# Optimization experiments

Measured on AMD Instinct MI355X. Metric: run time of the kernel, lower is better.

The kernel has to match this reference:

```python
import jax, jax.numpy as jnp
import numpy as np

EMBED_DIM = 1024
NUM_HEADS = 16
HEAD_DIM = EMBED_DIM // NUM_HEADS
BATCH = 2
SEQ = 2048


def setup_inputs() -> dict:
    key = jax.random.key(0)
    ks = jax.random.split(key, 10)
    s = 1.0 / np.sqrt(EMBED_DIM)
    inp = {
        "query": jax.random.normal(ks[0], (BATCH, SEQ, EMBED_DIM), jnp.float32),
        # Linear weights stored as [in, out] (y = x @ W + b)
        "wq": jax.random.normal(ks[1], (EMBED_DIM, EMBED_DIM), jnp.float32) * s,
        "bq": jnp.zeros((EMBED_DIM,), jnp.float32),
        "wk": jax.random.normal(ks[2], (EMBED_DIM, EMBED_DIM), jnp.float32) * s,
        "bk": jnp.zeros((EMBED_DIM,), jnp.float32),
        "wv": jax.random.normal(ks[3], (EMBED_DIM, EMBED_DIM), jnp.float32) * s,
        "bv": jnp.zeros((EMBED_DIM,), jnp.float32),
        "wo": jax.random.normal(ks[4], (EMBED_DIM, EMBED_DIM), jnp.float32) * s,
        "bo": jnp.zeros((EMBED_DIM,), jnp.float32),
        "temperature": jnp.float32(HEAD_DIM),  # learnable temperature, init = head_dim
    }
    return inp


def reference(query, wq, bq, wk, bk, wv, bv, wo, bo, temperature):
    B, S, E = query.shape
    # self-attention: key = value = query
    Q = (query @ wq + bq).reshape(B, S, NUM_HEADS, HEAD_DIM).transpose(0, 2, 1, 3)
    K = (query @ wk + bk).reshape(B, S, NUM_HEADS, HEAD_DIM).transpose(0, 2, 1, 3)
    V = (query @ wv + bv).reshape(B, S, NUM_HEADS, HEAD_DIM).transpose(0, 2, 1, 3)
    # squared Euclidean distances: ||q||^2 + ||k||^2 - 2<q,k>
    q_sq = jnp.sum(Q * Q, axis=-1, keepdims=True)          # (B,H,Sq,1)
    k_sq = jnp.sum(K * K, axis=-1, keepdims=True)          # (B,H,Sk,1)
    qk = jnp.einsum("bhqd,bhkd->bhqk", Q, K)
    d_sq = jnp.maximum(q_sq + jnp.swapaxes(k_sq, -2, -1) - 2.0 * qk, 0.0)
    attn = jax.nn.softmax(-d_sq / temperature, axis=-1)    # (B,H,Sq,Sk)
    out = jnp.einsum("bhqk,bhkd->bhqd", attn, V)
    out = out.transpose(0, 2, 1, 3).reshape(B, S, E)
    return out @ wo + bo
```

## Files before the change

kernel.cpp:

```cpp
#include <hip/hip_runtime.h>
#include <stdint.h>
#include <stddef.h>


#define LOG2E 1.44269504088896f

typedef __attribute__((ext_vector_type(8))) short bf16x8;
typedef __attribute__((ext_vector_type(4))) float f32x4;
typedef __attribute__((ext_vector_type(4))) unsigned short u16x4;
typedef __attribute__((ext_vector_type(8))) unsigned short u16x8;

__device__ __forceinline__ unsigned short f2b(float f) {
  union { float f; unsigned int u; } x; x.f = f;
  unsigned int u = x.u;
  u += 0x7fffu + ((u >> 16) & 1u);
  return (unsigned short)(u >> 16);
}
__device__ __forceinline__ float b2f(unsigned short s) {
  union { unsigned int u; float f; } x; x.u = ((unsigned int)s) << 16;
  return x.f;
}
__device__ __forceinline__ unsigned int fbits(float f) {
  union { float f; unsigned int u; } x; x.f = f; return x.u;
}

#define GLD_LDS(g, l) __builtin_amdgcn_global_load_lds( \
    (const __attribute__((address_space(1))) void*)(g), \
    (__attribute__((address_space(3))) void*)(l), 16, 0, 0)

__global__ void prep_kernel(const float* __restrict__ X,
                            const float* __restrict__ wq, const float* __restrict__ wk,
                            const float* __restrict__ wv, const float* __restrict__ wo,
                            unsigned short* __restrict__ Xb,
                            unsigned short* __restrict__ WTqkv, unsigned short* __restrict__ WTo) {
  int z = blockIdx.z;
  if (z == 4) {
    size_t base = ((size_t)(blockIdx.y * 16 + blockIdx.x)) * 16384;
    #pragma unroll
    for (int j = 0; j < 16; ++j) {
      size_t i = base + (size_t)(j * 256 + threadIdx.x) * 4;
      f32x4 v = *(const f32x4*)&X[i];
      u16x4 o;
      #pragma unroll
      for (int k = 0; k < 4; ++k) o[k] = f2b(v[k]);
      *(u16x4*)&Xb[i] = o;
    }
    return;
  }
  __shared__ float tile[64][65];
  const float* src = (z == 0) ? wq : (z == 1) ? wk : (z == 2) ? wv : wo;
  unsigned short* dst = (z < 3) ? (WTqkv + (size_t)z * 1024 * 1024) : WTo;
  int k0 = blockIdx.y * 64, n0 = blockIdx.x * 64;
  int rr = threadIdx.x >> 6, cc = threadIdx.x & 63;
  #pragma unroll
  for (int p = 0; p < 16; ++p) {
    int row = p * 4 + rr;
    tile[row][cc] = src[(size_t)(k0 + row) * 1024 + n0 + cc];
  }
  __syncthreads();
  #pragma unroll
  for (int p = 0; p < 16; ++p) {
    int row = p * 4 + rr;
    dst[(size_t)(n0 + row) * 1024 + k0 + cc] = f2b(tile[cc][row]);
  }
}

__global__ __launch_bounds__(256, 3) void gemm_qkv_kernel(
    const unsigned short* __restrict__ X, const unsigned short* __restrict__ WT,
    const float* __restrict__ bq, const float* __restrict__ bk, const float* __restrict__ bv,
    const float* __restrict__ temp,
    unsigned short* __restrict__ Qb, unsigned short* __restrict__ Kb,
    unsigned short* __restrict__ VTo, float* __restrict__ qs2, float* __restrict__ ks2) {
  __shared__ __align__(16) unsigned short smem[16896];
  unsigned short* As = smem;
  unsigned short* Bs = smem + 8192;
  const int t = threadIdx.x, w = t >> 6, lane = t & 63;
  const int r = lane & 15, q4 = lane >> 4;
  const int m0 = blockIdx.y * 128, n0 = blockIdx.x * 128;
  const int wr = (w >> 1) * 64, wc = (w & 1) * 64;
  const unsigned short* Xg = X + (size_t)m0 * 1024;
  const unsigned short* Wg = WT + (size_t)n0 * 1024;
  f32x4 acc[4][4] = {};
  for (int k0 = 0; k0 < 1024; k0 += 64) {
    #pragma unroll
    for (int g = 0; g < 4; ++g) {
      int slot = g * 256 + t;
      int kh = slot >> 9, row = (slot >> 2) & 127, ko = (slot & 3) * 8;
      GLD_LDS(Xg + (size_t)row * 1024 + k0 + kh * 32 + ko, &As[(g * 256 + w * 64) * 8]);
      GLD_LDS(Wg + (size_t)row * 1024 + k0 + kh * 32 + ko, &Bs[(g * 256 + w * 64) * 8]);
    }
    __syncthreads();
    #pragma unroll
    for (int kh = 0; kh < 2; ++kh) {
      bf16x8 af[4], bfr[4];
      #pragma unroll
      for (int mf = 0; mf < 4; ++mf)
        af[mf] = *(const bf16x8*)&As[kh * 4096 + (wr + mf * 16 + r) * 32 + q4 * 8];
      #pragma unroll
      for (int nf = 0; nf < 4; ++nf)
        bfr[nf] = *(const bf16x8*)&Bs[kh * 4096 + (wc + nf * 16 + r) * 32 + q4 * 8];
      #pragma unroll
      for (int mf = 0; mf < 4; ++mf)
        #pragma unroll
        for (int nf = 0; nf < 4; ++nf)
          acc[mf][nf] = __builtin_amdgcn_mfma_f32_16x16x32_bf16(af[mf], bfr[nf], acc[mf][nf], 0, 0, 0);
    }
    __syncthreads();
  }
  const int nblk = n0 >> 10;
  if (nblk < 2) {
    const float* bias = (nblk == 0) ? bq : bk;
    unsigned short* OutB = (nblk == 0) ? Qb : Kb;
    float* S2 = (nblk == 0) ? qs2 : ks2;
    const float sc = LOG2E / temp[0];
    const int nc0 = n0 & 1023;
    float s2a[4][4] = {};
    #pragma unroll
    for (int nf = 0; nf < 4; ++nf) {
      int n = nc0 + wc + nf * 16 + r;
      float bb = bias[n];
      #pragma unroll
      for (int mf = 0; mf < 4; ++mf) {
        int m = m0 + wr + mf * 16 + q4 * 4;
        f32x4 v = acc[mf][nf];
        #pragma unroll
        for (int i = 0; i < 4; ++i) {
          unsigned short os = f2b(v[i] + bb);
          OutB[(size_t)(m + i) * 1024 + n] = os;
          float xb = b2f(os);
          s2a[mf][i] += xb * xb;
        }
      }
    }
    #pragma unroll
    for (int mf = 0; mf < 4; ++mf)
      #pragma unroll
      for (int i = 0; i < 4; ++i) {
        float v = s2a[mf][i];
        v += __shfl_xor(v, 1, 64);
        v += __shfl_xor(v, 2, 64);
        v += __shfl_xor(v, 4, 64);
        v += __shfl_xor(v, 8, 64);
        s2a[mf][i] = v * sc;
      }
    if (r == 0) {
      int hh = (nc0 + wc) >> 6;
      #pragma unroll
      for (int mf = 0; mf < 4; ++mf) {
        int m = m0 + wr + mf * 16 + q4 * 4;
        int bb2 = m >> 11, ss = m & 2047;
        #pragma unroll
        for (int i = 0; i < 4; ++i)
          S2[(size_t)(bb2 * 16 + hh) * 2048 + ss + i] = s2a[mf][i];
      }
    }
  } else {
    unsigned short* Vt = smem;
    const int c0 = n0 - 2048;
    const int head = w & 1;
    #pragma unroll
    for (int nf = 0; nf < 4; ++nf) {
      int c = c0 + wc + nf * 16 + r;
      float bb = bv[c];
      int d = c & 63;
      #pragma unroll
      for (int mf = 0; mf < 4; ++mf) {
        int mloc = wr + mf * 16 + q4 * 4;
        int G = mloc >> 6;
        int k6 = mloc & 63;
        int pos = (k6 >> 5) * 32 + ((k6 & 15) >> 2) * 8 + ((k6 >> 4) & 1) * 4;
        f32x4 v = acc[mf][nf];
        u16x4 pk;
        #pragma unroll
        for (int i = 0; i < 4; ++i) pk[i] = f2b(v[i] + bb);
        *(u16x4*)&Vt[(head * 64 + d) * 132 + G * 64 + pos] = pk;
      }
    }
    __syncthreads();
    int row = t >> 1, ch = t & 1;
    int hd = row >> 6, dd = row & 63;
    int hglob = (c0 >> 6) + hd;
    int bb2 = m0 >> 11, s0 = m0 & 2047;
    unsigned short* dst = &VTo[((size_t)((bb2 * 16 + hglob) * 64 + dd)) * 2048 + s0 + ch * 64];
    const unsigned short* srcL = &Vt[(hd * 64 + dd) * 132 + ch * 64];
    #pragma unroll
    for (int k2 = 0; k2 < 16; ++k2)
      *(u16x4*)&dst[k2 * 4] = *(const u16x4*)&srcL[k2 * 4];
  }
}

__global__ __launch_bounds__(256, 2) void flash_kernel(
    const unsigned short* __restrict__ Qb, const unsigned short* __restrict__ Kb,
    const unsigned short* __restrict__ VT, const float* __restrict__ qs2,
    const float* __restrict__ ks2, const float* __restrict__ temp,
    unsigned short* __restrict__ AO) {
  __shared__ __align__(16) unsigned short Ks[2][64 * 64];
  __shared__ __align__(16) unsigned short Vs[2][64 * 64];
  const int t = threadIdx.x, w = t >> 6, lane = t & 63;
  const int r = lane & 15, q4 = lane >> 4;
  const int bh = blockIdx.y, b = bh >> 4, h = bh & 15;
  const int q0 = blockIdx.x * 128;
  const float cc = 2.0f * LOG2E / temp[0];

  bf16x8 qf[2][2];
  #pragma unroll
  for (int mf = 0; mf < 2; ++mf) {
    int sq = q0 + w * 32 + mf * 16 + r;
    const unsigned short* qp = Qb + (size_t)(b * 2048 + sq) * 1024 + h * 64;
    #pragma unroll
    for (int ks = 0; ks < 2; ++ks) qf[mf][ks] = *(const bf16x8*)(qp + ks * 32 + q4 * 8);
  }
  float qs_s[2];
  #pragma unroll
  for (int mf = 0; mf < 2; ++mf)
    qs_s[mf] = qs2[bh * 2048 + q0 + w * 32 + mf * 16 + r];

  f32x4 accO[2][4] = {};
  f32x4 lsum[2] = {};
  bf16x8 ones;
  #pragma unroll
  for (int j = 0; j < 8; ++j) ones[j] = (short)0x3F80;

  const unsigned short* Kg = Kb + ((size_t)b * 2048) * 1024 + h * 64;
  const unsigned short* Vg = VT + ((size_t)bh * 64) * 2048;
  const float* kqb = ks2 + bh * 2048;

  #pragma unroll
  for (int g = 0; g < 2; ++g) {
    int slot = g * 256 + t;
    int khalf = slot >> 8, key = (slot >> 2) & 63, ko = (slot & 3) * 8;
    GLD_LDS(Kg + (size_t)key * 1024 + khalf * 32 + ko, &Ks[0][slot * 8]);
    int dd = slot >> 3, pb = (slot & 7) ^ (dd & 7);
    GLD_LDS(Vg + (size_t)dd * 2048 + pb * 8, &Vs[0][slot * 8]);
  }
  f32x4 kq[4];
  #pragma unroll
  for (int kfm = 0; kfm < 4; ++kfm)
    kq[kfm] = *(const f32x4*)&kqb[kfm * 16 + q4 * 4];

  #pragma unroll 2
  for (int c = 0; c < 32; ++c) {
    const int buf = c & 1;
    __syncthreads();
    f32x4 kqn[4];
    if (c < 31) {
      #pragma unroll
      for (int g = 0; g < 2; ++g) {
        int slot = g * 256 + t;
        int khalf = slot >> 8, key = (slot >> 2) & 63, ko = (slot & 3) * 8;
        GLD_LDS(Kg + (size_t)((c + 1) * 64 + key) * 1024 + khalf * 32 + ko,
                &Ks[buf ^ 1][slot * 8]);
        int dd = slot >> 3, pb = (slot & 7) ^ (dd & 7);
        GLD_LDS(Vg + (size_t)dd * 2048 + (c + 1) * 64 + pb * 8,
                &Vs[buf ^ 1][slot * 8]);
      }
      #pragma unroll
      for (int kfm = 0; kfm < 4; ++kfm)
        kqn[kfm] = *(const f32x4*)&kqb[(c + 1) * 64 + kfm * 16 + q4 * 4];
    }

    f32x4 accST[4][2] = {};
    #pragma unroll
    for (int ks = 0; ks < 2; ++ks) {
      #pragma unroll
      for (int kfm = 0; kfm < 4; ++kfm) {
        bf16x8 ka = *(const bf16x8*)&Ks[buf][(ks * 64 + kfm * 16 + r) * 32 + q4 * 8];
        accST[kfm][0] = __builtin_amdgcn_mfma_f32_16x16x32_bf16(ka, qf[0][ks], accST[kfm][0], 0, 0, 0);
        accST[kfm][1] = __builtin_amdgcn_mfma_f32_16x16x32_bf16(ka, qf[1][ks], accST[kfm][1], 0, 0, 0);
      }
    }

    bf16x8 pf[2][2];
    #pragma unroll
    for (int cb = 0; cb < 2; ++cb) {
      #pragma unroll
      for (int mf = 0; mf < 2; ++mf) {
        unsigned int dw[4];
        #pragma unroll
        for (int half = 0; half < 2; ++half) {
          int kfm = cb * 2 + half;
          float pp[4];
          #pragma unroll
          for (int i = 0; i < 4; ++i) {
            float u = __builtin_fmaf(cc, accST[kfm][mf][i], -(kq[kfm][i] + qs_s[mf]));
            pp[i] = __builtin_amdgcn_exp2f(fminf(u, 0.f));
          }
          dw[half * 2 + 0] = (fbits(pp[0]) >> 16) | (fbits(pp[1]) & 0xFFFF0000u);
          dw[half * 2 + 1] = (fbits(pp[2]) >> 16) | (fbits(pp[3]) & 0xFFFF0000u);
        }
        union { unsigned int d[4]; bf16x8 v; } cv;
        cv.d[0] = dw[0]; cv.d[1] = dw[1]; cv.d[2] = dw[2]; cv.d[3] = dw[3];
        pf[cb][mf] = cv.v;
      }
    }

    #pragma unroll
    for (int cb = 0; cb < 2; ++cb) {
      #pragma unroll
      for (int mf = 0; mf < 2; ++mf)
        lsum[mf] = __builtin_amdgcn_mfma_f32_16x16x32_bf16(pf[cb][mf], ones, lsum[mf], 0, 0, 0);
      #pragma unroll
      for (int df = 0; df < 4; ++df) {
        int dloc = df * 16 + r;
        int un = dloc * 8 + ((cb * 4 + q4) ^ (dloc & 7));
        bf16x8 vb = *(const bf16x8*)&Vs[buf][un * 8];
        #pragma unroll
        for (int mf = 0; mf < 2; ++mf)
          accO[mf][df] = __builtin_amdgcn_mfma_f32_16x16x32_bf16(pf[cb][mf], vb, accO[mf][df], 0, 0, 0);
      }
    }
    if (c < 31) {
      #pragma unroll
      for (int kfm = 0; kfm < 4; ++kfm) kq[kfm] = kqn[kfm];
    }
  }
  #pragma unroll
  for (int mf = 0; mf < 2; ++mf) {
    float inv[4];
    #pragma unroll
    for (int i = 0; i < 4; ++i) inv[i] = 1.0f / lsum[mf][i];
    #pragma unroll
    for (int df = 0; df < 4; ++df) {
      int d = df * 16 + r;
      #pragma unroll
      for (int i = 0; i < 4; ++i) {
        int sq = q0 + w * 32 + mf * 16 + q4 * 4 + i;
        AO[(size_t)(b * 2048 + sq) * 1024 + h * 64 + d] = f2b(accO[mf][df][i] * inv[i]);
      }
    }
  }
}

__global__ __launch_bounds__(256, 2) void gemm_out_kernel(
    const unsigned short* __restrict__ A, const unsigned short* __restrict__ WT,
    const float* __restrict__ bo, float* __restrict__ Out) {
  __shared__ __align__(16) unsigned short As[2 * 128 * 32];
  __shared__ __align__(16) unsigned short Bs[2 * 64 * 32];
  const int t = threadIdx.x, w = t >> 6, lane = t & 63;
  const int r = lane & 15, q4 = lane >> 4;
  const int m0 = blockIdx.y * 128, n0 = blockIdx.x * 64;
  const int wr = (w >> 1) * 64, wc = (w & 1) * 32;
  const unsigned short* Ag = A + (size_t)m0 * 1024;
  const unsigned short* Wg = WT + (size_t)n0 * 1024;
  f32x4 acc[4][2] = {};
  for (int k0 = 0; k0 < 1024; k0 += 64) {
    #pragma unroll
    for (int g = 0; g < 4; ++g) {
      int slot = g * 256 + t;
      int kh = slot >> 9, row = (slot >> 2) & 127, ko = (slot & 3) * 8;
      GLD_LDS(Ag + (size_t)row * 1024 + k0 + kh * 32 + ko, &As[(g * 256 + w * 64) * 8]);
    }
    #pragma unroll
    for (int g = 0; g < 2; ++g) {
      int slot = g * 256 + t;
      int kh = slot >> 8, row = (slot >> 2) & 63, ko = (slot & 3) * 8;
      GLD_LDS(Wg + (size_t)row * 1024 + k0 + kh * 32 + ko, &Bs[(g * 256 + w * 64) * 8]);
    }
    __syncthreads();
    #pragma unroll
    for (int kh = 0; kh < 2; ++kh) {
      bf16x8 af[4], bfr[2];
      #pragma unroll
      for (int mf = 0; mf < 4; ++mf)
        af[mf] = *(const bf16x8*)&As[kh * 4096 + (wr + mf * 16 + r) * 32 + q4 * 8];
      #pragma unroll
      for (int nf = 0; nf < 2; ++nf)
        bfr[nf] = *(const bf16x8*)&Bs[kh * 2048 + (wc + nf * 16 + r) * 32 + q4 * 8];
      #pragma unroll
      for (int mf = 0; mf < 4; ++mf)
        #pragma unroll
        for (int nf = 0; nf < 2; ++nf)
          acc[mf][nf] = __builtin_amdgcn_mfma_f32_16x16x32_bf16(af[mf], bfr[nf], acc[mf][nf], 0, 0, 0);
    }
    __syncthreads();
  }
  #pragma unroll
  for (int nf = 0; nf < 2; ++nf) {
    int n = n0 + wc + nf * 16 + r;
    float bb = bo[n];
    #pragma unroll
    for (int mf = 0; mf < 4; ++mf) {
      int m = m0 + wr + mf * 16 + q4 * 4;
      f32x4 v = acc[mf][nf];
      #pragma unroll
      for (int i = 0; i < 4; ++i)
        Out[(size_t)(m + i) * 1024 + n] = v[i] + bb;
    }
  }
}

extern "C" void kernel_launch(void* const* d_in, const int* in_sizes, int n_in,
                              void* d_out, int out_size, void* d_ws, size_t ws_size,
                              hipStream_t stream) {
  const float* X    = (const float*)d_in[0];
  const float* wq   = (const float*)d_in[1];
  const float* bq   = (const float*)d_in[2];
  const float* wk   = (const float*)d_in[3];
  const float* bk   = (const float*)d_in[4];
  const float* wv   = (const float*)d_in[5];
  const float* bv   = (const float*)d_in[6];
  const float* wo   = (const float*)d_in[7];
  const float* bo   = (const float*)d_in[8];
  const float* temp = (const float*)d_in[9];
  float* Out = (float*)d_out;

  char* ws = (char*)d_ws;
  unsigned short* Xb    = (unsigned short*)ws; ws += (size_t)4096 * 1024 * 2;
  unsigned short* WTqkv = (unsigned short*)ws; ws += (size_t)3072 * 1024 * 2;
  unsigned short* WTo   = (unsigned short*)ws; ws += (size_t)1024 * 1024 * 2;
  unsigned short* Qb    = (unsigned short*)ws; ws += (size_t)4096 * 1024 * 2;
  unsigned short* Kb    = (unsigned short*)ws; ws += (size_t)4096 * 1024 * 2;
  unsigned short* VT    = (unsigned short*)ws; ws += (size_t)4096 * 1024 * 2;
  float* qs2 = (float*)ws; ws += (size_t)65536 * 4;
  float* ks2 = (float*)ws; ws += (size_t)65536 * 4;
  unsigned short* AO = Xb;

  prep_kernel<<<dim3(16, 16, 5), 256, 0, stream>>>(X, wq, wk, wv, wo, Xb, WTqkv, WTo);
  gemm_qkv_kernel<<<dim3(24, 32), 256, 0, stream>>>(Xb, WTqkv, bq, bk, bv, temp, Qb, Kb, VT, qs2, ks2);
  flash_kernel<<<dim3(16, 32), 256, 0, stream>>>(Qb, Kb, VT, qs2, ks2, temp, AO);
  gemm_out_kernel<<<dim3(16, 32), 256, 0, stream>>>(AO, WTo, bo, Out);
}
```

Before: 203.2 us.

## Double-buffer GEMM k-loops and drop per-row q-norm term from softmax

The QKV and output projection GEMMs now use a double-buffered LDS pipeline with 32-wide k-steps and a single barrier per step, prefetching the next tile during compute. The per-query squared norm is dropped because it is constant across keys and cancels in the softmax, which removes the qs2 buffer, its loads and the clamp before exp2. The flash kernel load addressing is simplified to incrementing pointers. Removing the clamp relies on exponents staying bounded, and skipping the row-max subtraction could overflow for larger-magnitude inputs.

```diff
diff --git a/kernel.cpp b/kernel.cpp
--- a/kernel.cpp
+++ b/kernel.cpp
@@ -8,7 +8,6 @@
 typedef __attribute__((ext_vector_type(8))) short bf16x8;
 typedef __attribute__((ext_vector_type(4))) float f32x4;
 typedef __attribute__((ext_vector_type(4))) unsigned short u16x4;
-typedef __attribute__((ext_vector_type(8))) unsigned short u16x8;
 
 __device__ __forceinline__ unsigned short f2b(float f) {
   union { float f; unsigned int u; } x; x.f = f;
@@ -70,7 +69,7 @@
     const float* __restrict__ bq, const float* __restrict__ bk, const float* __restrict__ bv,
     const float* __restrict__ temp,
     unsigned short* __restrict__ Qb, unsigned short* __restrict__ Kb,
-    unsigned short* __restrict__ VTo, float* __restrict__ qs2, float* __restrict__ ks2) {
+    unsigned short* __restrict__ VTo, float* __restrict__ ks2) {
   __shared__ __align__(16) unsigned short smem[16896];
   unsigned short* As = smem;
   unsigned short* Bs = smem + 8192;
@@ -80,45 +79,63 @@
   const int wr = (w >> 1) * 64, wc = (w & 1) * 64;
   const unsigned short* Xg = X + (size_t)m0 * 1024;
   const unsigned short* Wg = WT + (size_t)n0 * 1024;
+  const unsigned short* xp0 = Xg + (size_t)(t >> 2) * 1024 + (t & 3) * 8;
+  const unsigned short* xp1 = xp0 + (size_t)64 * 1024;
+  const unsigned short* wp0 = Wg + (size_t)(t >> 2) * 1024 + (t & 3) * 8;
+  const unsigned short* wp1 = wp0 + (size_t)64 * 1024;
   f32x4 acc[4][4] = {};
-  for (int k0 = 0; k0 < 1024; k0 += 64) {
-    #pragma unroll
-    for (int g = 0; g < 4; ++g) {
-      int slot = g * 256 + t;
-      int kh = slot >> 9, row = (slot >> 2) & 127, ko = (slot & 3) * 8;
-      GLD_LDS(Xg + (size_t)row * 1024 + k0 + kh * 32 + ko, &As[(g * 256 + w * 64) * 8]);
-      GLD_LDS(Wg + (size_t)row * 1024 + k0 + kh * 32 + ko, &Bs[(g * 256 + w * 64) * 8]);
-    }
+  GLD_LDS(xp0, &As[t * 8]);
+  GLD_LDS(xp1, &As[(256 + t) * 8]);
+  GLD_LDS(wp0, &Bs[t * 8]);
+  GLD_LDS(wp1, &Bs[(256 + t) * 8]);
+  #pragma unroll 2
+  for (int kk = 0; kk < 32; ++kk) {
+    const int buf = kk & 1;
     __syncthreads();
-    #pragma unroll
-    for (int kh = 0; kh < 2; ++kh) {
-      bf16x8 af[4], bfr[4];
-      #pragma unroll
-      for (int mf = 0; mf < 4; ++mf)
-        af[mf] = *(const bf16x8*)&As[kh * 4096 + (wr + mf * 16 + r) * 32 + q4 * 8];
+    if (kk < 31) {
+      int ko = (kk + 1) * 32;
+      GLD_LDS(xp0 + ko, &As[(buf ^ 1) * 4096 + t * 8]);
+      GLD_LDS(xp1 + ko, &As[(buf ^ 1) * 4096 + (256 + t) * 8]);
+      GLD_LDS(wp0 + ko, &Bs[(buf ^ 1) * 4096 + t * 8]);
+      GLD_LDS(wp1 + ko, &Bs[(buf ^ 1) * 4096 + (256 + t) * 8]);
+    }
+    bf16x8 af[4], bfr[4];
+    #pragma unroll
+    for (int mf = 0; mf < 4; ++mf)
+      af[mf] = *(const bf16x8*)&As[buf * 4096 + (wr + mf * 16 + r) * 32 + q4 * 8];
+    #pragma unroll
+    for (int nf = 0; nf < 4; ++nf)
+      bfr[nf] = *(const bf16x8*)&Bs[buf * 4096 + (wc + nf * 16 + r) * 32 + q4 * 8];
+    #pragma unroll
+    for (int mf = 0; mf < 4; ++mf)
       #pragma unroll
       for (int nf = 0; nf < 4; ++nf)
-        bfr[nf] = *(const bf16x8*)&Bs[kh * 4096 + (wc + nf * 16 + r) * 32 + q4 * 8];
-      #pragma unroll
-      for (int mf = 0; mf < 4; ++mf)
-        #pragma unroll
-        for (int nf = 0; nf < 4; ++nf)
-          acc[mf][nf] = __builtin_amdgcn_mfma_f32_16x16x32_bf16(af[mf], bfr[nf], acc[mf][nf], 0, 0, 0);
-    }
-    __syncthreads();
+        acc[mf][nf] = __builtin_amdgcn_mfma_f32_16x16x32_bf16(af[mf], bfr[nf], acc[mf][nf], 0, 0, 0);
   }
   const int nblk = n0 >> 10;
-  if (nblk < 2) {
-    const float* bias = (nblk == 0) ? bq : bk;
-    unsigned short* OutB = (nblk == 0) ? Qb : Kb;
-    float* S2 = (nblk == 0) ? qs2 : ks2;
+  if (nblk == 0) {
+    const int nc0 = n0 & 1023;
+    #pragma unroll
+    for (int nf = 0; nf < 4; ++nf) {
+      int n = nc0 + wc + nf * 16 + r;
+      float bb = bq[n];
+      #pragma unroll
+      for (int mf = 0; mf < 4; ++mf) {
+        int m = m0 + wr + mf * 16 + q4 * 4;
+        f32x4 v = acc[mf][nf];
+        #pragma unroll
+        for (int i = 0; i < 4; ++i)
+          Qb[(size_t)(m + i) * 1024 + n] = f2b(v[i] + bb);
+      }
+    }
+  } else if (nblk == 1) {
     const float sc = LOG2E / temp[0];
     const int nc0 = n0 & 1023;
     float s2a[4][4] = {};
     #pragma unroll
     for (int nf = 0; nf < 4; ++nf) {
       int n = nc0 + wc + nf * 16 + r;
-      float bb = bias[n];
+      float bb = bk[n];
       #pragma unroll
       for (int mf = 0; mf < 4; ++mf) {
         int m = m0 + wr + mf * 16 + q4 * 4;
@@ -126,7 +143,7 @@
         #pragma unroll
         for (int i = 0; i < 4; ++i) {
           unsigned short os = f2b(v[i] + bb);
-          OutB[(size_t)(m + i) * 1024 + n] = os;
+          Kb[(size_t)(m + i) * 1024 + n] = os;
           float xb = b2f(os);
           s2a[mf][i] += xb * xb;
         }
@@ -151,10 +168,11 @@
         int bb2 = m >> 11, ss = m & 2047;
         #pragma unroll
         for (int i = 0; i < 4; ++i)
-          S2[(size_t)(bb2 * 16 + hh) * 2048 + ss + i] = s2a[mf][i];
+          ks2[(size_t)(bb2 * 16 + hh) * 2048 + ss + i] = s2a[mf][i];
       }
     }
   } else {
+    __syncthreads();
     unsigned short* Vt = smem;
     const int c0 = n0 - 2048;
     const int head = w & 1;
@@ -191,9 +209,8 @@
 
 __global__ __launch_bounds__(256, 2) void flash_kernel(
     const unsigned short* __restrict__ Qb, const unsigned short* __restrict__ Kb,
-    const unsigned short* __restrict__ VT, const float* __restrict__ qs2,
-    const float* __restrict__ ks2, const float* __restrict__ temp,
-    unsigned short* __restrict__ AO) {
+    const unsigned short* __restrict__ VT, const float* __restrict__ ks2,
+    const float* __restrict__ temp, unsigned short* __restrict__ AO) {
   __shared__ __align__(16) unsigned short Ks[2][64 * 64];
   __shared__ __align__(16) unsigned short Vs[2][64 * 64];
   const int t = threadIdx.x, w = t >> 6, lane = t & 63;
@@ -210,10 +227,6 @@
     #pragma unroll
     for (int ks = 0; ks < 2; ++ks) qf[mf][ks] = *(const bf16x8*)(qp + ks * 32 + q4 * 8);
   }
-  float qs_s[2];
-  #pragma unroll
-  for (int mf = 0; mf < 2; ++mf)
-    qs_s[mf] = qs2[bh * 2048 + q0 + w * 32 + mf * 16 + r];
 
   f32x4 accO[2][4] = {};
   f32x4 lsum[2] = {};
@@ -225,39 +238,32 @@
   const unsigned short* Vg = VT + ((size_t)bh * 64) * 2048;
   const float* kqb = ks2 + bh * 2048;
 
-  #pragma unroll
-  for (int g = 0; g < 2; ++g) {
-    int slot = g * 256 + t;
-    int khalf = slot >> 8, key = (slot >> 2) & 63, ko = (slot & 3) * 8;
-    GLD_LDS(Kg + (size_t)key * 1024 + khalf * 32 + ko, &Ks[0][slot * 8]);
-    int dd = slot >> 3, pb = (slot & 7) ^ (dd & 7);
-    GLD_LDS(Vg + (size_t)dd * 2048 + pb * 8, &Vs[0][slot * 8]);
-  }
-  f32x4 kq[4];
-  #pragma unroll
-  for (int kfm = 0; kfm < 4; ++kfm)
-    kq[kfm] = *(const f32x4*)&kqb[kfm * 16 + q4 * 4];
+  const unsigned short* kp0 = Kg + (size_t)(t >> 2) * 1024 + (t & 3) * 8;
+  const unsigned short* kp1 = kp0 + 32;
+  int dd0 = t >> 3;
+  const unsigned short* vp0 = Vg + (size_t)dd0 * 2048 + ((t & 7) ^ (dd0 & 7)) * 8;
+  const unsigned short* vp1 = vp0 + (size_t)32 * 2048;
+  GLD_LDS(kp0, &Ks[0][t * 8]);
+  GLD_LDS(kp1, &Ks[0][(256 + t) * 8]);
+  GLD_LDS(vp0, &Vs[0][t * 8]);
+  GLD_LDS(vp1, &Vs[0][(256 + t) * 8]);
+  kp0 += 65536; kp1 += 65536; vp0 += 64; vp1 += 64;
 
   #pragma unroll 2
   for (int c = 0; c < 32; ++c) {
     const int buf = c & 1;
     __syncthreads();
-    f32x4 kqn[4];
     if (c < 31) {
-      #pragma unroll
-      for (int g = 0; g < 2; ++g) {
-        int slot = g * 256 + t;
-        int khalf = slot >> 8, key = (slot >> 2) & 63, ko = (slot & 3) * 8;
-        GLD_LDS(Kg + (size_t)((c + 1) * 64 + key) * 1024 + khalf * 32 + ko,
-                &Ks[buf ^ 1][slot * 8]);
-        int dd = slot >> 3, pb = (slot & 7) ^ (dd & 7);
-        GLD_LDS(Vg + (size_t)dd * 2048 + (c + 1) * 64 + pb * 8,
-                &Vs[buf ^ 1][slot * 8]);
-      }
-      #pragma unroll
-      for (int kfm = 0; kfm < 4; ++kfm)
-        kqn[kfm] = *(const f32x4*)&kqb[(c + 1) * 64 + kfm * 16 + q4 * 4];
-    }
+      GLD_LDS(kp0, &Ks[buf ^ 1][t * 8]);
+      GLD_LDS(kp1, &Ks[buf ^ 1][(256 + t) * 8]);
+      GLD_LDS(vp0, &Vs[buf ^ 1][t * 8]);
+      GLD_LDS(vp1, &Vs[buf ^ 1][(256 + t) * 8]);
+      kp0 += 65536; kp1 += 65536; vp0 += 64; vp1 += 64;
+    }
+    f32x4 kq[4];
+    #pragma unroll
+    for (int kfm = 0; kfm < 4; ++kfm)
+      kq[kfm] = *(const f32x4*)&kqb[c * 64 + kfm * 16 + q4 * 4];
 
     f32x4 accST[4][2] = {};
     #pragma unroll
@@ -282,8 +288,8 @@
           float pp[4];
           #pragma unroll
           for (int i = 0; i < 4; ++i) {
-            float u = __builtin_fmaf(cc, accST[kfm][mf][i], -(kq[kfm][i] + qs_s[mf]));
-            pp[i] = __builtin_amdgcn_exp2f(fminf(u, 0.f));
+            float u = __builtin_fmaf(cc, accST[kfm][mf][i], -kq[kfm][i]);
+            pp[i] = __builtin_amdgcn_exp2f(u);
           }
           dw[half * 2 + 0] = (fbits(pp[0]) >> 16) | (fbits(pp[1]) & 0xFFFF0000u);
           dw[half * 2 + 1] = (fbits(pp[2]) >> 16) | (fbits(pp[3]) & 0xFFFF0000u);
@@ -309,10 +315,6 @@
           accO[mf][df] = __builtin_amdgcn_mfma_f32_16x16x32_bf16(pf[cb][mf], vb, accO[mf][df], 0, 0, 0);
       }
     }
-    if (c < 31) {
-      #pragma unroll
-      for (int kfm = 0; kfm < 4; ++kfm) kq[kfm] = kqn[kfm];
-    }
   }
   #pragma unroll
   for (int mf = 0; mf < 2; ++mf) {
@@ -334,45 +336,43 @@
 __global__ __launch_bounds__(256, 2) void gemm_out_kernel(
     const unsigned short* __restrict__ A, const unsigned short* __restrict__ WT,
     const float* __restrict__ bo, float* __restrict__ Out) {
-  __shared__ __align__(16) unsigned short As[2 * 128 * 32];
-  __shared__ __align__(16) unsigned short Bs[2 * 64 * 32];
+  __shared__ __align__(16) unsigned short As[2][128 * 32];
+  __shared__ __align__(16) unsigned short Bs[2][64 * 32];
   const int t = threadIdx.x, w = t >> 6, lane = t & 63;
   const int r = lane & 15, q4 = lane >> 4;
   const int m0 = blockIdx.y * 128, n0 = blockIdx.x * 64;
   const int wr = (w >> 1) * 64, wc = (w & 1) * 32;
   const unsigned short* Ag = A + (size_t)m0 * 1024;
   const unsigned short* Wg = WT + (size_t)n0 * 1024;
+  const unsigned short* ap0 = Ag + (size_t)(t >> 2) * 1024 + (t & 3) * 8;
+  const unsigned short* ap1 = ap0 + (size_t)64 * 1024;
+  const unsigned short* wp0 = Wg + (size_t)(t >> 2) * 1024 + (t & 3) * 8;
   f32x4 acc[4][2] = {};
-  for (int k0 = 0; k0 < 1024; k0 += 64) {
-    #pragma unroll
-    for (int g = 0; g < 4; ++g) {
-      int slot = g * 256 + t;
-      int kh = slot >> 9, row = (slot >> 2) & 127, ko = (slot & 3) * 8;
-      GLD_LDS(Ag + (size_t)row * 1024 + k0 + kh * 32 + ko, &As[(g * 256 + w * 64) * 8]);
-    }
-    #pragma unroll
-    for (int g = 0; g < 2; ++g) {
-      int slot = g * 256 + t;
-      int kh = slot >> 8, row = (slot >> 2) & 63, ko = (slot & 3) * 8;
-      GLD_LDS(Wg + (size_t)row * 1024 + k0 + kh * 32 + ko, &Bs[(g * 256 + w * 64) * 8]);
-    }
+  GLD_LDS(ap0, &As[0][t * 8]);
+  GLD_LDS(ap1, &As[0][(256 + t) * 8]);
+  GLD_LDS(wp0, &Bs[0][t * 8]);
+  #pragma unroll 2
+  for (int kk = 0; kk < 32; ++kk) {
+    const int buf = kk & 1;
     __syncthreads();
-    #pragma unroll
-    for (int kh = 0; kh < 2; ++kh) {
-      bf16x8 af[4], bfr[2];
-      #pragma unroll
-      for (int mf = 0; mf < 4; ++mf)
-        af[mf] = *(const bf16x8*)&As[kh * 4096 + (wr + mf * 16 + r) * 32 + q4 * 8];
+    if (kk < 31) {
+      int ko = (kk + 1) * 32;
+      GLD_LDS(ap0 + ko, &As[buf ^ 1][t * 8]);
+      GLD_LDS(ap1 + ko, &As[buf ^ 1][(256 + t) * 8]);
+      GLD_LDS(wp0 + ko, &Bs[buf ^ 1][t * 8]);
+    }
+    bf16x8 af[4], bfr[2];
+    #pragma unroll
+    for (int mf = 0; mf < 4; ++mf)
+      af[mf] = *(const bf16x8*)&As[buf][(wr + mf * 16 + r) * 32 + q4 * 8];
+    #pragma unroll
+    for (int nf = 0; nf < 2; ++nf)
+      bfr[nf] = *(const bf16x8*)&Bs[buf][(wc + nf * 16 + r) * 32 + q4 * 8];
+    #pragma unroll
+    for (int mf = 0; mf < 4; ++mf)
       #pragma unroll
       for (int nf = 0; nf < 2; ++nf)
-        bfr[nf] = *(const bf16x8*)&Bs[kh * 2048 + (wc + nf * 16 + r) * 32 + q4 * 8];
-      #pragma unroll
-      for (int mf = 0; mf < 4; ++mf)
-        #pragma unroll
-        for (int nf = 0; nf < 2; ++nf)
-          acc[mf][nf] = __builtin_amdgcn_mfma_f32_16x16x32_bf16(af[mf], bfr[nf], acc[mf][nf], 0, 0, 0);
-    }
-    __syncthreads();
+        acc[mf][nf] = __builtin_amdgcn_mfma_f32_16x16x32_bf16(af[mf], bfr[nf], acc[mf][nf], 0, 0, 0);
   }
   #pragma unroll
   for (int nf = 0; nf < 2; ++nf) {
@@ -411,12 +411,11 @@
   unsigned short* Qb    = (unsigned short*)ws; ws += (size_t)4096 * 1024 * 2;
   unsigned short* Kb    = (unsigned short*)ws; ws += (size_t)4096 * 1024 * 2;
   unsigned short* VT    = (unsigned short*)ws; ws += (size_t)4096 * 1024 * 2;
-  float* qs2 = (float*)ws; ws += (size_t)65536 * 4;
   float* ks2 = (float*)ws; ws += (size_t)65536 * 4;
   unsigned short* AO = Xb;
 
   prep_kernel<<<dim3(16, 16, 5), 256, 0, stream>>>(X, wq, wk, wv, wo, Xb, WTqkv, WTo);
-  gemm_qkv_kernel<<<dim3(24, 32), 256, 0, stream>>>(Xb, WTqkv, bq, bk, bv, temp, Qb, Kb, VT, qs2, ks2);
-  flash_kernel<<<dim3(16, 32), 256, 0, stream>>>(Qb, Kb, VT, qs2, ks2, temp, AO);
+  gemm_qkv_kernel<<<dim3(24, 32), 256, 0, stream>>>(Xb, WTqkv, bq, bk, bv, temp, Qb, Kb, VT, ks2);
+  flash_kernel<<<dim3(16, 32), 256, 0, stream>>>(Qb, Kb, VT, ks2, temp, AO);
   gemm_out_kernel<<<dim3(16, 32), 256, 0, stream>>>(AO, WTo, bo, Out);
 }
```

Measured after the change: 207.5 us. +2.1%, slower.

## Load K/V tiles straight to registers and drop the query-norm softmax term

Applied to the files above, without the earlier changes.

The flash kernel no longer stages K and V tiles in double-buffered LDS with barriers. Each wave now reads its K and V MFMA fragments directly from global memory into registers, which removes the syncthreads and LDS traffic but makes the four waves in a block fetch the same data redundantly. Separately, the per-query squared-norm term is dropped from the exponent, relying on softmax shift invariance, and the clamp to non-positive values is removed. The QKV GEMM therefore no longer computes or stores q_sq. Without that term and the clamp, the exponent is no longer bounded above, so overflow protection now depends on the input scale.

```diff
diff --git a/kernel.cpp b/kernel.cpp
--- a/kernel.cpp
+++ b/kernel.cpp
@@ -8,7 +8,6 @@
 typedef __attribute__((ext_vector_type(8))) short bf16x8;
 typedef __attribute__((ext_vector_type(4))) float f32x4;
 typedef __attribute__((ext_vector_type(4))) unsigned short u16x4;
-typedef __attribute__((ext_vector_type(8))) unsigned short u16x8;
 
 __device__ __forceinline__ unsigned short f2b(float f) {
   union { float f; unsigned int u; } x; x.f = f;
@@ -70,7 +69,7 @@
     const float* __restrict__ bq, const float* __restrict__ bk, const float* __restrict__ bv,
     const float* __restrict__ temp,
     unsigned short* __restrict__ Qb, unsigned short* __restrict__ Kb,
-    unsigned short* __restrict__ VTo, float* __restrict__ qs2, float* __restrict__ ks2) {
+    unsigned short* __restrict__ VTo, float* __restrict__ ks2) {
   __shared__ __align__(16) unsigned short smem[16896];
   unsigned short* As = smem;
   unsigned short* Bs = smem + 8192;
@@ -108,17 +107,29 @@
     __syncthreads();
   }
   const int nblk = n0 >> 10;
-  if (nblk < 2) {
-    const float* bias = (nblk == 0) ? bq : bk;
-    unsigned short* OutB = (nblk == 0) ? Qb : Kb;
-    float* S2 = (nblk == 0) ? qs2 : ks2;
+  if (nblk == 0) {
+    const int nc0 = n0 & 1023;
+    #pragma unroll
+    for (int nf = 0; nf < 4; ++nf) {
+      int n = nc0 + wc + nf * 16 + r;
+      float bb = bq[n];
+      #pragma unroll
+      for (int mf = 0; mf < 4; ++mf) {
+        int m = m0 + wr + mf * 16 + q4 * 4;
+        f32x4 v = acc[mf][nf];
+        #pragma unroll
+        for (int i = 0; i < 4; ++i)
+          Qb[(size_t)(m + i) * 1024 + n] = f2b(v[i] + bb);
+      }
+    }
+  } else if (nblk == 1) {
     const float sc = LOG2E / temp[0];
     const int nc0 = n0 & 1023;
     float s2a[4][4] = {};
     #pragma unroll
     for (int nf = 0; nf < 4; ++nf) {
       int n = nc0 + wc + nf * 16 + r;
-      float bb = bias[n];
+      float bb = bk[n];
       #pragma unroll
       for (int mf = 0; mf < 4; ++mf) {
         int m = m0 + wr + mf * 16 + q4 * 4;
@@ -126,7 +137,7 @@
         #pragma unroll
         for (int i = 0; i < 4; ++i) {
           unsigned short os = f2b(v[i] + bb);
-          OutB[(size_t)(m + i) * 1024 + n] = os;
+          Kb[(size_t)(m + i) * 1024 + n] = os;
           float xb = b2f(os);
           s2a[mf][i] += xb * xb;
         }
@@ -151,7 +162,7 @@
         int bb2 = m >> 11, ss = m & 2047;
         #pragma unroll
         for (int i = 0; i < 4; ++i)
-          S2[(size_t)(bb2 * 16 + hh) * 2048 + ss + i] = s2a[mf][i];
+          ks2[(size_t)(bb2 * 16 + hh) * 2048 + ss + i] = s2a[mf][i];
       }
     }
   } else {
@@ -191,11 +202,8 @@
 
 __global__ __launch_bounds__(256, 2) void flash_kernel(
     const unsigned short* __restrict__ Qb, const unsigned short* __restrict__ Kb,
-    const unsigned short* __restrict__ VT, const float* __restrict__ qs2,
-    const float* __restrict__ ks2, const float* __restrict__ temp,
-    unsigned short* __restrict__ AO) {
-  __shared__ __align__(16) unsigned short Ks[2][64 * 64];
-  __shared__ __align__(16) unsigned short Vs[2][64 * 64];
+    const unsigned short* __restrict__ VT, const float* __restrict__ ks2,
+    const float* __restrict__ temp, unsigned short* __restrict__ AO) {
   const int t = threadIdx.x, w = t >> 6, lane = t & 63;
   const int r = lane & 15, q4 = lane >> 4;
   const int bh = blockIdx.y, b = bh >> 4, h = bh & 15;
@@ -210,10 +218,6 @@
     #pragma unroll
     for (int ks = 0; ks < 2; ++ks) qf[mf][ks] = *(const bf16x8*)(qp + ks * 32 + q4 * 8);
   }
-  float qs_s[2];
-  #pragma unroll
-  for (int mf = 0; mf < 2; ++mf)
-    qs_s[mf] = qs2[bh * 2048 + q0 + w * 32 + mf * 16 + r];
 
   f32x4 accO[2][4] = {};
   f32x4 lsum[2] = {};
@@ -221,52 +225,38 @@
   #pragma unroll
   for (int j = 0; j < 8; ++j) ones[j] = (short)0x3F80;
 
-  const unsigned short* Kg = Kb + ((size_t)b * 2048) * 1024 + h * 64;
-  const unsigned short* Vg = VT + ((size_t)bh * 64) * 2048;
-  const float* kqb = ks2 + bh * 2048;
-
-  #pragma unroll
-  for (int g = 0; g < 2; ++g) {
-    int slot = g * 256 + t;
-    int khalf = slot >> 8, key = (slot >> 2) & 63, ko = (slot & 3) * 8;
-    GLD_LDS(Kg + (size_t)key * 1024 + khalf * 32 + ko, &Ks[0][slot * 8]);
-    int dd = slot >> 3, pb = (slot & 7) ^ (dd & 7);
-    GLD_LDS(Vg + (size_t)dd * 2048 + pb * 8, &Vs[0][slot * 8]);
-  }
-  f32x4 kq[4];
-  #pragma unroll
-  for (int kfm = 0; kfm < 4; ++kfm)
-    kq[kfm] = *(const f32x4*)&kqb[kfm * 16 + q4 * 4];
+  const unsigned short* kp0 = Kb + ((size_t)b * 2048 + r) * 1024 + h * 64 + q4 * 8;
+  const unsigned short* kp1 = kp0 + 16 * 1024;
+  const unsigned short* kp2 = kp0 + 32 * 1024;
+  const unsigned short* kp3 = kp0 + 48 * 1024;
+  const unsigned short* vp0 = VT + ((size_t)bh * 64 + r) * 2048 + q4 * 8;
+  const unsigned short* vp1 = vp0 + (size_t)16 * 2048;
+  const unsigned short* vp2 = vp0 + (size_t)32 * 2048;
+  const unsigned short* vp3 = vp0 + (size_t)48 * 2048;
+  const float* kqp = ks2 + bh * 2048 + q4 * 4;
 
   #pragma unroll 2
   for (int c = 0; c < 32; ++c) {
-    const int buf = c & 1;
-    __syncthreads();
-    f32x4 kqn[4];
-    if (c < 31) {
-      #pragma unroll
-      for (int g = 0; g < 2; ++g) {
-        int slot = g * 256 + t;
-        int khalf = slot >> 8, key = (slot >> 2) & 63, ko = (slot & 3) * 8;
-        GLD_LDS(Kg + (size_t)((c + 1) * 64 + key) * 1024 + khalf * 32 + ko,
-                &Ks[buf ^ 1][slot * 8]);
-        int dd = slot >> 3, pb = (slot & 7) ^ (dd & 7);
-        GLD_LDS(Vg + (size_t)dd * 2048 + (c + 1) * 64 + pb * 8,
-                &Vs[buf ^ 1][slot * 8]);
-      }
-      #pragma unroll
-      for (int kfm = 0; kfm < 4; ++kfm)
-        kqn[kfm] = *(const f32x4*)&kqb[(c + 1) * 64 + kfm * 16 + q4 * 4];
-    }
+    bf16x8 ka[2][4], vb[2][4];
+    ka[0][0] = *(const bf16x8*)(kp0);      ka[1][0] = *(const bf16x8*)(kp0 + 32);
+    ka[0][1] = *(const bf16x8*)(kp1);      ka[1][1] = *(const bf16x8*)(kp1 + 32);
+    ka[0][2] = *(const bf16x8*)(kp2);      ka[1][2] = *(const bf16x8*)(kp2 + 32);
+    ka[0][3] = *(const bf16x8*)(kp3);      ka[1][3] = *(const bf16x8*)(kp3 + 32);
+    vb[0][0] = *(const bf16x8*)(vp0);      vb[1][0] = *(const bf16x8*)(vp0 + 32);
+    vb[0][1] = *(const bf16x8*)(vp1);      vb[1][1] = *(const bf16x8*)(vp1 + 32);
+    vb[0][2] = *(const bf16x8*)(vp2);      vb[1][2] = *(const bf16x8*)(vp2 + 32);
+    vb[0][3] = *(const bf16x8*)(vp3);      vb[1][3] = *(const bf16x8*)(vp3 + 32);
+    f32x4 kq[4];
+    #pragma unroll
+    for (int kfm = 0; kfm < 4; ++kfm) kq[kfm] = *(const f32x4*)(kqp + kfm * 16);
 
     f32x4 accST[4][2] = {};
     #pragma unroll
     for (int ks = 0; ks < 2; ++ks) {
       #pragma unroll
       for (int kfm = 0; kfm < 4; ++kfm) {
-        bf16x8 ka = *(const bf16x8*)&Ks[buf][(ks * 64 + kfm * 16 + r) * 32 + q4 * 8];
-        accST[kfm][0] = __builtin_amdgcn_mfma_f32_16x16x32_bf16(ka, qf[0][ks], accST[kfm][0], 0, 0, 0);
-        accST[kfm][1] = __builtin_amdgcn_mfma_f32_16x16x32_bf16(ka, qf[1][ks], accST[kfm][1], 0, 0, 0);
+        accST[kfm][0] = __builtin_amdgcn_mfma_f32_16x16x32_bf16(ka[ks][kfm], qf[0][ks], accST[kfm][0], 0, 0, 0);
+        accST[kfm][1] = __builtin_amdgcn_mfma_f32_16x16x32_bf16(ka[ks][kfm], qf[1][ks], accST[kfm][1], 0, 0, 0);
       }
     }
 
@@ -282,8 +272,8 @@
           float pp[4];
           #pragma unroll
           for (int i = 0; i < 4; ++i) {
-            float u = __builtin_fmaf(cc, accST[kfm][mf][i], -(kq[kfm][i] + qs_s[mf]));
-            pp[i] = __builtin_amdgcn_exp2f(fminf(u, 0.f));
+            float u = __builtin_fmaf(cc, accST[kfm][mf][i], -kq[kfm][i]);
+            pp[i] = __builtin_amdgcn_exp2f(u);
           }
           dw[half * 2 + 0] = (fbits(pp[0]) >> 16) | (fbits(pp[1]) & 0xFFFF0000u);
           dw[half * 2 + 1] = (fbits(pp[2]) >> 16) | (fbits(pp[3]) & 0xFFFF0000u);
@@ -301,18 +291,14 @@
         lsum[mf] = __builtin_amdgcn_mfma_f32_16x16x32_bf16(pf[cb][mf], ones, lsum[mf], 0, 0, 0);
       #pragma unroll
       for (int df = 0; df < 4; ++df) {
-        int dloc = df * 16 + r;
-        int un = dloc * 8 + ((cb * 4 + q4) ^ (dloc & 7));
-        bf16x8 vb = *(const bf16x8*)&Vs[buf][un * 8];
         #pragma unroll
         for (int mf = 0; mf < 2; ++mf)
-          accO[mf][df] = __builtin_amdgcn_mfma_f32_16x16x32_bf16(pf[cb][mf], vb, accO[mf][df], 0, 0, 0);
-      }
-    }
-    if (c < 31) {
-      #pragma unroll
-      for (int kfm = 0; kfm < 4; ++kfm) kq[kfm] = kqn[kfm];
-    }
+          accO[mf][df] = __builtin_amdgcn_mfma_f32_16x16x32_bf16(pf[cb][mf], vb[cb][df], accO[mf][df], 0, 0, 0);
+      }
+    }
+    kp0 += 65536; kp1 += 65536; kp2 += 65536; kp3 += 65536;
+    vp0 += 64; vp1 += 64; vp2 += 64; vp3 += 64;
+    kqp += 64;
   }
   #pragma unroll
   for (int mf = 0; mf < 2; ++mf) {
@@ -411,12 +397,11 @@
   unsigned short* Qb    = (unsigned short*)ws; ws += (size_t)4096 * 1024 * 2;
   unsigned short* Kb    = (unsigned short*)ws; ws += (size_t)4096 * 1024 * 2;
   unsigned short* VT    = (unsigned short*)ws; ws += (size_t)4096 * 1024 * 2;
-  float* qs2 = (float*)ws; ws += (size_t)65536 * 4;
   float* ks2 = (float*)ws; ws += (size_t)65536 * 4;
   unsigned short* AO = Xb;
 
   prep_kernel<<<dim3(16, 16, 5), 256, 0, stream>>>(X, wq, wk, wv, wo, Xb, WTqkv, WTo);
-  gemm_qkv_kernel<<<dim3(24, 32), 256, 0, stream>>>(Xb, WTqkv, bq, bk, bv, temp, Qb, Kb, VT, qs2, ks2);
-  flash_kernel<<<dim3(16, 32), 256, 0, stream>>>(Qb, Kb, VT, qs2, ks2, temp, AO);
+  gemm_qkv_kernel<<<dim3(24, 32), 256, 0, stream>>>(Xb, WTqkv, bq, bk, bv, temp, Qb, Kb, VT, ks2);
+  flash_kernel<<<dim3(16, 32), 256, 0, stream>>>(Qb, Kb, VT, ks2, temp, AO);
   gemm_out_kernel<<<dim3(16, 32), 256, 0, stream>>>(AO, WTo, bo, Out);
 }
```

Result: slower. 287.3 us (+41.4%).
